# Optimization experiments

Hardware: AMD Instinct MI355X
Metric: run time of the kernel (lower is better)

The kernel has to match this reference:

```python
import jax, jax.numpy as jnp
import numpy as np

B, K, W, H = 32, 64, 100, 150
ALPHA = 0.2        # leaky-relu slope
THRES = 2e-4       # causal threshold


def setup_inputs() -> dict:
    ks = jax.random.split(jax.random.key(0), 20)
    s = 0.1
    inp = {
        "x": jax.random.normal(ks[0], (B, K, W), jnp.float32),
        "y": jax.random.normal(ks[1], (B, K, 1), jnp.float32),
        "z_noise": jax.random.normal(ks[2], (B, H), jnp.float32),
        "lin_w": jax.random.normal(ks[3], (W, W), jnp.float32) * s,
        "lin_b": jax.random.normal(ks[4], (W,), jnp.float32) * s,
        "a": jax.random.normal(ks[5], (2, 1), jnp.float32),
        "bias": jax.random.normal(ks[6], (K, K * W), jnp.float32) * 0.01,
        "gl_wih": jax.random.normal(ks[7], (3 * H, W), jnp.float32) * s,
        "gl_whh": jax.random.normal(ks[8], (3 * H, H), jnp.float32) * s,
        "gl_bih": jax.random.normal(ks[9], (3 * H,), jnp.float32) * s,
        "gl_bhh": jax.random.normal(ks[10], (3 * H,), jnp.float32) * s,
        "mu_w": jax.random.normal(ks[11], (H, H), jnp.float32) * s,
        "mu_b": jax.random.normal(ks[12], (H,), jnp.float32) * s,
        "std_w": jax.random.normal(ks[13], (H, H), jnp.float32) * s,
        "std_b": jax.random.normal(ks[14], (H,), jnp.float32) * s,
        "net_wih": jax.random.normal(ks[15], (K, 3 * H, W), jnp.float32) * s,
        "net_whh": jax.random.normal(ks[16], (K, 3 * H, H), jnp.float32) * s,
        "net_bih": jax.random.normal(ks[17], (K, 3 * H), jnp.float32) * s,
        "net_bhh": jax.random.normal(ks[18], (K, 3 * H), jnp.float32) * s,
    }
    return inp


def _gru_last(wih, whh, bih, bhh, xs, h0):
    # xs: [B, S, in], h0: [B, H] -> final hidden [B, H]. PyTorch gate order r,z,n.
    gx = jnp.einsum('bsi,gi->sbg', xs, wih) + bih  # [S, B, 3H]
    h_dim = h0.shape[-1]

    def step(h, g):
        gh = h @ whh.T + bhh
        r = jax.nn.sigmoid(g[:, :h_dim] + gh[:, :h_dim])
        z = jax.nn.sigmoid(g[:, h_dim:2 * h_dim] + gh[:, h_dim:2 * h_dim])
        n = jnp.tanh(g[:, 2 * h_dim:] + r * gh[:, 2 * h_dim:])
        return (1.0 - z) * n + z * h, None

    h_last, _ = jax.lax.scan(step, h0, gx)
    return h_last


def reference(x, y, z_noise, lin_w, lin_b, a, bias, gl_wih, gl_whh, gl_bih, gl_bhh,
              mu_w, mu_b, std_w, std_b, net_wih, net_whh, net_bih, net_bhh):
    xw = x[:, :, -W:]
    Wx = xw @ lin_w.T + lin_b                       # [B, K, W]
    v = Wx.reshape(Wx.shape[0], K * W)              # [B, K*W]
    # e = a_input @ a, where a_input[...,0]=y broadcast, a_input[...,1]=v tiled per node
    e = a[0, 0] * y + a[1, 0] * v[:, None, :] + bias  # [B, K, K*W]
    e = jax.nn.leaky_relu(e, ALPHA)
    attention = jax.nn.softmax(e, axis=2)           # dropout p=0 -> identity
    A = attention >= THRES                           # [B, K, K*W] mask
    Ax = jnp.where(A, v[:, None, :], 0.0)
    cause_x = Wx + Ax.sum(axis=2, keepdims=True)    # [B, K, W]
    # left GRU over the node dimension (seq len = K)
    h0 = jnp.zeros((cause_x.shape[0], H), cause_x.dtype)
    h_t = _gru_last(gl_wih, gl_whh, gl_bih, gl_bhh, cause_x, h0)  # [B, H]
    mu = h_t @ mu_w.T + mu_b
    log_var = h_t @ std_w.T + std_b
    sigma = jnp.exp(0.5 * log_var)
    z = mu + sigma * z_noise                        # [B, H]
    # K independent GRUs, same input Wx and same init state z -> vmap over weights
    causes = jax.vmap(lambda wi, wh, bi, bh: _gru_last(wi, wh, bi, bh, Wx, z))(
        net_wih, net_whh, net_bih, net_bhh)         # [K, B, H]
    return causes.transpose(1, 0, 2)                # [B, K, H]
```

## Files before the change

### kernel.cpp

```cpp
#include <hip/hip_runtime.h>

#define Bc 32
#define Kc 64
#define Wc 100
#define Hc 150
#define H3c 450
#define KWc 6400
#define ALPHAc 0.2f
#define THRESc 0.0002f

typedef unsigned int u32;
typedef unsigned short u16;
typedef __attribute__((ext_vector_type(8))) short short8;
typedef __attribute__((ext_vector_type(4))) float floatx4;

#define OFF_WX      0u
#define OFF_CS      204800u
#define OFF_GX      206848u
#define OFF_HT      1128448u
#define OFF_Z       1133248u

__device__ __forceinline__ float us2f(u16 u){ u32 x=((u32)u)<<16; return __uint_as_float(x); }
__device__ __forceinline__ u16 f2us(float f){
  u32 x = __float_as_uint(f);
  u32 r = (x + 0x7fffu + ((x>>16)&1u)) >> 16;
  return (u16)r;
}

__device__ __forceinline__ void lds_barrier(){
  __builtin_amdgcn_sched_barrier(0);
  asm volatile("s_waitcnt lgkmcnt(0)" ::: "memory");
  __builtin_amdgcn_s_barrier();
  __builtin_amdgcn_sched_barrier(0);
}

__global__ void wx_kernel(const float* __restrict__ x, const float* __restrict__ lin_w,
                          const float* __restrict__ lin_b, float* __restrict__ ws){
  int o = blockIdx.x*256 + threadIdx.x;
  if (o >= Bc*KWc) return;
  int i = o % Wc;
  int bk = o / Wc;
  const float4* xr = (const float4*)(x + bk*Wc);
  const float4* wr = (const float4*)(lin_w + i*Wc);
  float acc = lin_b[i];
  #pragma unroll
  for (int j=0;j<25;j++){
    float4 xv = xr[j], wv = wr[j];
    acc += xv.x*wv.x + xv.y*wv.y + xv.z*wv.z + xv.w*wv.w;
  }
  ws[OFF_WX + o] = acc;
}

__global__ void attn_kernel(const float* __restrict__ y, const float* __restrict__ a,
                            const float* __restrict__ bias, float* __restrict__ ws){
  __shared__ __align__(16) float e_l[KWc];
  __shared__ float red[4];
  int row = blockIdx.x;
  int b = row >> 6, k = row & 63;
  int tid = threadIdx.x;
  float a0 = a[0], a1 = a[1];
  float yv = y[row];
  const float4* v4  = (const float4*)(ws + OFF_WX + (size_t)b*KWc);
  const float4* br4 = (const float4*)(bias + (size_t)k*KWc);
  float4* e4 = (float4*)e_l;
  float ay = a0*yv;
  float m = -3.4e38f;
  for (int j=tid; j<KWc/4; j+=256){
    float4 vv = v4[j], bb = br4[j];
    float4 e;
    e.x = ay + a1*vv.x + bb.x; e.x = (e.x>=0.f)?e.x:ALPHAc*e.x;
    e.y = ay + a1*vv.y + bb.y; e.y = (e.y>=0.f)?e.y:ALPHAc*e.y;
    e.z = ay + a1*vv.z + bb.z; e.z = (e.z>=0.f)?e.z:ALPHAc*e.z;
    e.w = ay + a1*vv.w + bb.w; e.w = (e.w>=0.f)?e.w:ALPHAc*e.w;
    e4[j] = e;
    m = fmaxf(m, fmaxf(fmaxf(e.x,e.y), fmaxf(e.z,e.w)));
  }
  for (int o=32;o;o>>=1) m = fmaxf(m, __shfl_down(m, o));
  if ((tid&63)==0) red[tid>>6] = m;
  __syncthreads();
  m = fmaxf(fmaxf(red[0],red[1]), fmaxf(red[2],red[3]));
  __syncthreads();
  float ssum = 0.f;
  for (int j=tid; j<KWc/4; j+=256){
    float4 e = e4[j];
    ssum += __expf(e.x-m) + __expf(e.y-m) + __expf(e.z-m) + __expf(e.w-m);
  }
  for (int o=32;o;o>>=1) ssum += __shfl_down(ssum, o);
  if ((tid&63)==0) red[tid>>6] = ssum;
  __syncthreads();
  float s = red[0]+red[1]+red[2]+red[3];
  float thr = m + logf(THRESc * s);
  float cs = 0.f;
  for (int j=tid; j<KWc/4; j+=256){
    float4 e = e4[j];
    float4 vv = v4[j];
    if (e.x >= thr) cs += vv.x;
    if (e.y >= thr) cs += vv.y;
    if (e.z >= thr) cs += vv.z;
    if (e.w >= thr) cs += vv.w;
  }
  for (int o=32;o;o>>=1) cs += __shfl_down(cs, o);
  if ((tid&63)==0) red[tid>>6] = cs;
  __syncthreads();
  if (tid==0) ws[OFF_CS + row] = red[0]+red[1]+red[2]+red[3];
}

__global__ void glproj_kernel(const float* __restrict__ gl_wih, const float* __restrict__ gl_bih,
                              float* __restrict__ ws){
  int o = blockIdx.x*256 + threadIdx.x;
  if (o >= Kc*Bc*H3c) return;
  int g = o % H3c;
  int t = o / H3c;
  int b = t & 31, s = t >> 5;
  float cs = ws[OFF_CS + b*Kc + s];
  const float4* xr = (const float4*)(ws + OFF_WX + b*KWc + s*Wc);
  const float4* wr = (const float4*)(gl_wih + g*Wc);
  float acc = gl_bih[g];
  #pragma unroll
  for (int j=0;j<25;j++){
    float4 wv = wr[j], xv = xr[j];
    acc += (xv.x+cs)*wv.x + (xv.y+cs)*wv.y + (xv.z+cs)*wv.z + (xv.w+cs)*wv.w;
  }
  ws[OFF_GX + o] = acc;
}

__global__ void __launch_bounds__(512,1) glgru4_kernel(
    const float* __restrict__ gl_whh, const float* __restrict__ gl_bhh,
    float* __restrict__ ws){
  __shared__ __align__(16) float hbuf[2][152];
  __shared__ float dotb[3*152];
  int b = blockIdx.x;
  int tid = threadIdx.x;
  bool dotter = (tid < 450);
  int g = dotter ? tid/150 : 0;
  int t = dotter ? (tid - g*150) : 0;

  u32 wreg[75];
  {
    const float* wr = gl_whh + (size_t)(g*Hc + t)*Hc;
    #pragma unroll
    for (int k2=0;k2<75;k2++){
      float2 wv = dotter ? *(const float2*)(wr + 2*k2) : make_float2(0.f,0.f);
      wreg[k2] = (u32)f2us(wv.x) | ((u32)f2us(wv.y) << 16);
    }
  }
  if (tid < 152){ hbuf[0][tid] = 0.f; hbuf[1][tid] = 0.f; }

  float bh_r=0.f, bh_z=0.f, bh_n=0.f, hreg=0.f;
  if (tid < Hc){
    bh_r = gl_bhh[tid]; bh_z = gl_bhh[Hc+tid]; bh_n = gl_bhh[2*Hc+tid];
  }
  __syncthreads();

  for (int s=0;s<Kc;s++){
    int rb = s & 1;
    float gxr=0.f, gxz=0.f, gxn=0.f;
    if (tid < Hc){
      const float* gp = ws + OFF_GX + (size_t)(s*Bc + b)*H3c;
      gxr = gp[tid]; gxz = gp[Hc+tid]; gxn = gp[2*Hc+tid];
    }
    if (dotter){
      const float* hb = hbuf[rb];
      float a0=0.f, a1=0.f, a2=0.f;
      #pragma unroll
      for (int k2=0;k2<75;k2+=3){
        u32 u0 = wreg[k2], u1 = wreg[k2+1], u2 = wreg[k2+2];
        float2 h0 = *(const float2*)(hb + 2*k2);
        float2 h1 = *(const float2*)(hb + 2*k2+2);
        float2 h2 = *(const float2*)(hb + 2*k2+4);
        a0 += __uint_as_float(u0<<16)*h0.x + __uint_as_float(u0&0xffff0000u)*h0.y;
        a1 += __uint_as_float(u1<<16)*h1.x + __uint_as_float(u1&0xffff0000u)*h1.y;
        a2 += __uint_as_float(u2<<16)*h2.x + __uint_as_float(u2&0xffff0000u)*h2.y;
      }
      dotb[g*152 + t] = a0 + a1 + a2;
    }
    lds_barrier();
    if (tid < Hc){
      float a_r = gxr + dotb[tid]       + bh_r;
      float a_z = gxz + dotb[152+tid]   + bh_z;
      float dn  =       dotb[304+tid]   + bh_n;
      float rr = 1.f/(1.f+__expf(-a_r));
      float zz = 1.f/(1.f+__expf(-a_z));
      float nx = gxn + rr*dn;
      nx = fminf(fmaxf(nx,-15.f),15.f);
      float e2 = __expf(2.f*nx);
      float n = (e2-1.f)/(e2+1.f);
      float h = (1.f-zz)*n + zz*hreg;
      hreg = h;
      hbuf[rb^1][tid] = h;
    }
    lds_barrier();
  }
  if (tid < Hc) ws[OFF_HT + (size_t)b*Hc + tid] = hreg;
}

__global__ void z_kernel(const float* __restrict__ z_noise, const float* __restrict__ mu_w,
                         const float* __restrict__ mu_b, const float* __restrict__ std_w,
                         const float* __restrict__ std_b, float* __restrict__ ws){
  int o = blockIdx.x*256 + threadIdx.x;
  if (o >= Bc*Hc) return;
  int t = o % Hc, b = o / Hc;
  const float* h = ws + OFF_HT + b*Hc;
  const float2* mwr = (const float2*)(mu_w + t*Hc);
  const float2* swr = (const float2*)(std_w + t*Hc);
  float mu = mu_b[t], lv = std_b[t];
  for (int j=0;j<Hc/2;j++){
    float2 mw = mwr[j], sw = swr[j];
    float h0 = h[2*j], h1 = h[2*j+1];
    mu += h0*mw.x + h1*mw.y;
    lv += h0*sw.x + h1*sw.y;
  }
  float sg = expf(0.5f*lv);
  ws[OFF_Z + o] = mu + sg*z_noise[o];
}

__global__ void __launch_bounds__(512,1) causes3_kernel(
    const float* __restrict__ net_wih, const float* __restrict__ net_whh,
    const float* __restrict__ net_bih, const float* __restrict__ net_bhh,
    const float* __restrict__ ws, float* __restrict__ out){
  __shared__ __align__(16) u16 bF[9*16*40];
  __shared__ float g_rz[320*10];
  __shared__ float g_nh[160*10];
  __shared__ float g_np[160*10];
  int kk = blockIdx.x & 63, bg = blockIdx.x >> 6, b0 = bg*8;
  int tid = threadIdx.x;
  int w = tid >> 6, lane = tid & 63, quad = lane >> 4, n16 = lane & 15;
  const float* whhk = net_whh + (size_t)kk*H3c*Hc;
  const float* wihk = net_wih + (size_t)kk*H3c*Wc;
  const float* bihk = net_bih + kk*H3c;
  const float* bhhk = net_bhh + kk*H3c;

  short8 whhA[4][5], wihA[4][4];
  #pragma unroll
  for (int ti=0; ti<4; ti++){
    int tile = w*4 + ti;
    int sec = tile/10;
    int sr = (tile - sec*10)*16 + n16;
    bool rowok = (tile < 30) && (sr < Hc);
    int grow = (sec<3 ? sec : 2)*Hc + sr;
    #pragma unroll
    for (int c=0;c<5;c++){
      union { short8 v; u16 u[8]; } t8;
      #pragma unroll
      for (int j=0;j<8;j++){
        int k = c*32 + quad*8 + j;
        float v = (rowok && k < Hc) ? whhk[(size_t)grow*Hc + k] : 0.f;
        t8.u[j] = f2us(v);
      }
      whhA[ti][c] = t8.v;
    }
    #pragma unroll
    for (int c=0;c<4;c++){
      union { short8 v; u16 u[8]; } t8;
      #pragma unroll
      for (int j=0;j<8;j++){
        int k = c*32 + quad*8 + j;
        float v = (rowok && k < Wc) ? wihk[(size_t)grow*Wc + k] : 0.f;
        t8.u[j] = f2us(v);
      }
      wihA[ti][c] = t8.v;
    }
  }

  for (int i=tid; i<9*16*40/2; i+=512) ((u32*)bF)[i] = 0u;

  float hst[3] = {0.f,0.f,0.f};
  float brz_r[3], brz_z[3], bnh_[3], bnp_[3];
  #pragma unroll
  for (int q=0;q<3;q++){
    int task = tid + q*512;
    if (task < 1200){
      int t = task >> 3, bb = task & 7;
      float h = ws[OFF_Z + (b0+bb)*Hc + t];
      hst[q] = h;
      brz_r[q] = bhhk[t]      + bihk[t];
      brz_z[q] = bhhk[Hc+t]   + bihk[Hc+t];
      bnh_[q]  = bhhk[2*Hc+t];
      bnp_[q]  = bihk[2*Hc+t];
      u16 hi = f2us(h); float hif = us2f(hi); u16 lo = f2us(h - hif);
      bF[(t>>5)*640 + bb*40 + (t&31)] = hi;
      bF[(t>>5)*640 + (bb+8)*40 + (t&31)] = lo;
    }
  }
  for (int it=tid; it<800; it+=512){
    int bb = it/100, i = it - bb*100;
    float xv = ws[OFF_WX + (b0+bb)*KWc + i];
    bF[(5+(i>>5))*640 + bb*40 + (i&31)] = f2us(xv);
  }

  int bb0 = tid/100, i0 = tid - bb0*100;
  int it1 = tid + 512;
  int bb1 = it1/100, i1 = it1 - bb1*100;
  bool v1ok = (it1 < 800);

  const bool isN = (w >= 5);
  for (int s=0;s<Kc;s++){
    float xp0 = 0.f, xp1 = 0.f;
    if (s < Kc-1){
      xp0 = ws[OFF_WX + (size_t)(b0+bb0)*KWc + (s+1)*Wc + i0];
      if (v1ok) xp1 = ws[OFF_WX + (size_t)(b0+bb1)*KWc + (s+1)*Wc + i1];
    }
    lds_barrier();
    const u16* bBase = bF + (size_t)n16*40 + (size_t)quad*8;
    short8 bx[4];
    #pragma unroll
    for (int c=0;c<4;c++) bx[c] = *(const short8*)(bBase + (size_t)(5+c)*640);
    short8 bh[5];
    #pragma unroll
    for (int c=0;c<5;c++) bh[c] = *(const short8*)(bBase + (size_t)c*640);
    floatx4 acc[4] = {{0.f,0.f,0.f,0.f},{0.f,0.f,0.f,0.f},{0.f,0.f,0.f,0.f},{0.f,0.f,0.f,0.f}};
    #pragma unroll
    for (int ca=0;ca<4;ca++){
      #pragma unroll
      for (int ti=0;ti<4;ti++)
        acc[ti] = __builtin_amdgcn_mfma_f32_16x16x32_bf16(wihA[ti][ca], bx[ca], acc[ti], 0,0,0);
    }
    if (isN){
      if (n16 < 8){
        #pragma unroll
        for (int ti=0;ti<4;ti++){
          int tile = w*4 + ti;
          if (tile < 30){
            int srb = (tile - 20)*16 + quad*4;
            float* gq = g_np + srb*10 + n16;
            #pragma unroll
            for (int r=0;r<4;r++) gq[r*10] = acc[ti][r];
          }
        }
      }
      #pragma unroll
      for (int ti=0;ti<4;ti++) acc[ti] = (floatx4){0.f,0.f,0.f,0.f};
    }
    #pragma unroll
    for (int c=0;c<5;c++){
      #pragma unroll
      for (int ti=0;ti<4;ti++)
        acc[ti] = __builtin_amdgcn_mfma_f32_16x16x32_bf16(whhA[ti][c], bh[c], acc[ti], 0,0,0);
    }
    #pragma unroll
    for (int ti=0;ti<4;ti++){
      #pragma unroll
      for (int r=0;r<4;r++) acc[ti][r] += __shfl_xor(acc[ti][r], 8);
    }
    if (n16 < 8){
      #pragma unroll
      for (int ti=0;ti<4;ti++){
        int tile = w*4 + ti;
        if (tile < 30){
          int sec = tile/10;
          int srb = (tile - sec*10)*16 + quad*4;
          if (sec < 2){
            float* gp = g_rz + (sec*160 + srb)*10 + n16;
            #pragma unroll
            for (int r=0;r<4;r++) gp[r*10] = acc[ti][r];
          } else {
            float* gh = g_nh + srb*10 + n16;
            #pragma unroll
            for (int r=0;r<4;r++) gh[r*10] = acc[ti][r];
          }
        }
      }
    }
    lds_barrier();
    #pragma unroll
    for (int q=0;q<3;q++){
      int task = tid + q*512;
      if (task < 1200){
        int t = task >> 3, bb = task & 7;
        float a_r = g_rz[t*10+bb] + brz_r[q];
        float a_z = g_rz[(160+t)*10+bb] + brz_z[q];
        float r  = 1.f/(1.f+__expf(-a_r));
        float zz = 1.f/(1.f+__expf(-a_z));
        float nx = (g_np[t*10+bb] + bnp_[q]) + r*(g_nh[t*10+bb] + bnh_[q]);
        nx = fminf(fmaxf(nx,-15.f),15.f);
        float e2 = __expf(2.f*nx);
        float n = (e2-1.f)/(e2+1.f);
        float h = (1.f-zz)*n + zz*hst[q];
        hst[q] = h;
        u16 hi = f2us(h); float hif = us2f(hi); u16 lo = f2us(h - hif);
        bF[(t>>5)*640 + bb*40 + (t&31)] = hi;
        bF[(t>>5)*640 + (bb+8)*40 + (t&31)] = lo;
      }
    }
    if (s < Kc-1){
      bF[(5+(i0>>5))*640 + bb0*40 + (i0&31)] = f2us(xp0);
      if (v1ok) bF[(5+(i1>>5))*640 + bb1*40 + (i1&31)] = f2us(xp1);
    }
  }
  #pragma unroll
  for (int q=0;q<3;q++){
    int task = tid + q*512;
    if (task < 1200){
      int t = task >> 3, bb = task & 7;
      out[((size_t)(b0+bb)*Kc + kk)*Hc + t] = hst[q];
    }
  }
}

extern "C" void kernel_launch(void* const* d_in, const int* in_sizes, int n_in,
                              void* d_out, int out_size, void* d_ws, size_t ws_size,
                              hipStream_t stream){
  const float* x        = (const float*)d_in[0];
  const float* y        = (const float*)d_in[1];
  const float* z_noise  = (const float*)d_in[2];
  const float* lin_w    = (const float*)d_in[3];
  const float* lin_b    = (const float*)d_in[4];
  const float* a        = (const float*)d_in[5];
  const float* bias     = (const float*)d_in[6];
  const float* gl_wih   = (const float*)d_in[7];
  const float* gl_whh   = (const float*)d_in[8];
  const float* gl_bih   = (const float*)d_in[9];
  const float* gl_bhh   = (const float*)d_in[10];
  const float* mu_w     = (const float*)d_in[11];
  const float* mu_b     = (const float*)d_in[12];
  const float* std_w    = (const float*)d_in[13];
  const float* std_b    = (const float*)d_in[14];
  const float* net_wih  = (const float*)d_in[15];
  const float* net_whh  = (const float*)d_in[16];
  const float* net_bih  = (const float*)d_in[17];
  const float* net_bhh  = (const float*)d_in[18];
  float* ws = (float*)d_ws;
  float* out = (float*)d_out;

  wx_kernel<<<(Bc*KWc+255)/256, 256, 0, stream>>>(x, lin_w, lin_b, ws);
  attn_kernel<<<Bc*Kc, 256, 0, stream>>>(y, a, bias, ws);
  glproj_kernel<<<(Kc*Bc*H3c+255)/256, 256, 0, stream>>>(gl_wih, gl_bih, ws);
  glgru4_kernel<<<Bc, 512, 0, stream>>>(gl_whh, gl_bhh, ws);
  z_kernel<<<(Bc*Hc+255)/256, 256, 0, stream>>>(z_noise, mu_w, mu_b, std_w, std_b, ws);
  causes3_kernel<<<Kc*4, 512, 0, stream>>>(net_wih, net_whh, net_bih, net_bhh, ws, out);
}
```

Baseline: 483.8 us.

## Split left-GRU recurrent dot across 1024 threads and fuse z projection

The left GRU kernel now uses 900 active threads, so each hidden-row dot product is split into two halves that are summed through LDS. Its recurrent weights are kept in fp32 registers instead of packed bf16. The mu/log-var projection and reparameterisation are folded into the end of the same kernel, which removes the separate z_kernel launch. Shorter per-step dot chains should cut latency in the 64-step serial loop, at the cost of more threads, more registers per thread and an extra LDS add per gate.

```diff
diff --git a/kernel.cpp b/kernel.cpp
--- a/kernel.cpp
+++ b/kernel.cpp
@@ -124,25 +124,30 @@
   ws[OFF_GX + o] = acc;
 }
 
-__global__ void __launch_bounds__(512,1) glgru4_kernel(
+__global__ void __launch_bounds__(1024,1) glgru4_kernel(
     const float* __restrict__ gl_whh, const float* __restrict__ gl_bhh,
-    float* __restrict__ ws){
+    const float* __restrict__ z_noise, const float* __restrict__ mu_w,
+    const float* __restrict__ mu_b, const float* __restrict__ std_w,
+    const float* __restrict__ std_b, float* __restrict__ ws){
   __shared__ __align__(16) float hbuf[2][152];
-  __shared__ float dotb[3*152];
+  __shared__ __align__(16) float dotb[2][3][152];
   int b = blockIdx.x;
   int tid = threadIdx.x;
-  bool dotter = (tid < 450);
-  int g = dotter ? tid/150 : 0;
-  int t = dotter ? (tid - g*150) : 0;
-
-  u32 wreg[75];
-  {
-    const float* wr = gl_whh + (size_t)(g*Hc + t)*Hc;
-    #pragma unroll
-    for (int k2=0;k2<75;k2++){
-      float2 wv = dotter ? *(const float2*)(wr + 2*k2) : make_float2(0.f,0.f);
-      wreg[k2] = (u32)f2us(wv.x) | ((u32)f2us(wv.y) << 16);
-    }
+  bool dotter = (tid < 900);
+  int half = (tid >= 450) ? 1 : 0;
+  int row  = dotter ? (tid - half*450) : 0;
+  int g = row/150, t = row - g*150;
+
+  float wreg[76];
+  if (dotter){
+    const float* wr = gl_whh + (size_t)row*Hc + half*76;
+    #pragma unroll
+    for (int i=0;i<37;i++){
+      float2 v = *(const float2*)(wr + 2*i);
+      wreg[2*i] = v.x; wreg[2*i+1] = v.y;
+    }
+    if (!half){ float2 v = *(const float2*)(wr + 74); wreg[74]=v.x; wreg[75]=v.y; }
+    else      { wreg[74]=0.f; wreg[75]=0.f; }
   }
   if (tid < 152){ hbuf[0][tid] = 0.f; hbuf[1][tid] = 0.f; }
 
@@ -160,28 +165,28 @@
       gxr = gp[tid]; gxz = gp[Hc+tid]; gxn = gp[2*Hc+tid];
     }
     if (dotter){
-      const float* hb = hbuf[rb];
-      float a0=0.f, a1=0.f, a2=0.f;
-      #pragma unroll
-      for (int k2=0;k2<75;k2+=3){
-        u32 u0 = wreg[k2], u1 = wreg[k2+1], u2 = wreg[k2+2];
-        float2 h0 = *(const float2*)(hb + 2*k2);
-        float2 h1 = *(const float2*)(hb + 2*k2+2);
-        float2 h2 = *(const float2*)(hb + 2*k2+4);
-        a0 += __uint_as_float(u0<<16)*h0.x + __uint_as_float(u0&0xffff0000u)*h0.y;
-        a1 += __uint_as_float(u1<<16)*h1.x + __uint_as_float(u1&0xffff0000u)*h1.y;
-        a2 += __uint_as_float(u2<<16)*h2.x + __uint_as_float(u2&0xffff0000u)*h2.y;
-      }
-      dotb[g*152 + t] = a0 + a1 + a2;
+      const float* hb = &hbuf[rb][half*76];
+      float a0=0.f,a1=0.f,a2=0.f,a3=0.f;
+      #pragma unroll
+      for (int i=0;i<19;i++){
+        float4 h4 = *(const float4*)(hb + 4*i);
+        a0 += wreg[4*i]  *h4.x;
+        a1 += wreg[4*i+1]*h4.y;
+        a2 += wreg[4*i+2]*h4.z;
+        a3 += wreg[4*i+3]*h4.w;
+      }
+      dotb[half][g][t] = (a0+a1)+(a2+a3);
     }
     lds_barrier();
     if (tid < Hc){
-      float a_r = gxr + dotb[tid]       + bh_r;
-      float a_z = gxz + dotb[152+tid]   + bh_z;
-      float dn  =       dotb[304+tid]   + bh_n;
+      float dr = dotb[0][0][tid] + dotb[1][0][tid];
+      float dz = dotb[0][1][tid] + dotb[1][1][tid];
+      float dn = dotb[0][2][tid] + dotb[1][2][tid];
+      float a_r = gxr + dr + bh_r;
+      float a_z = gxz + dz + bh_z;
       float rr = 1.f/(1.f+__expf(-a_r));
       float zz = 1.f/(1.f+__expf(-a_z));
-      float nx = gxn + rr*dn;
+      float nx = gxn + rr*(dn + bh_n);
       nx = fminf(fmaxf(nx,-15.f),15.f);
       float e2 = __expf(2.f*nx);
       float n = (e2-1.f)/(e2+1.f);
@@ -192,26 +197,26 @@
     lds_barrier();
   }
   if (tid < Hc) ws[OFF_HT + (size_t)b*Hc + tid] = hreg;
-}
-
-__global__ void z_kernel(const float* __restrict__ z_noise, const float* __restrict__ mu_w,
-                         const float* __restrict__ mu_b, const float* __restrict__ std_w,
-                         const float* __restrict__ std_b, float* __restrict__ ws){
-  int o = blockIdx.x*256 + threadIdx.x;
-  if (o >= Bc*Hc) return;
-  int t = o % Hc, b = o / Hc;
-  const float* h = ws + OFF_HT + b*Hc;
-  const float2* mwr = (const float2*)(mu_w + t*Hc);
-  const float2* swr = (const float2*)(std_w + t*Hc);
-  float mu = mu_b[t], lv = std_b[t];
-  for (int j=0;j<Hc/2;j++){
-    float2 mw = mwr[j], sw = swr[j];
-    float h0 = h[2*j], h1 = h[2*j+1];
-    mu += h0*mw.x + h1*mw.y;
-    lv += h0*sw.x + h1*sw.y;
-  }
-  float sg = expf(0.5f*lv);
-  ws[OFF_Z + o] = mu + sg*z_noise[o];
+
+  if (tid < 300){
+    int which = tid/150, tt = tid - which*150;
+    const float* wrow = (which ? std_w : mu_w) + (size_t)tt*Hc;
+    float acc = which ? std_b[tt] : mu_b[tt];
+    const float* hb = hbuf[0];
+    #pragma unroll
+    for (int i=0;i<75;i++){
+      float2 wv = *(const float2*)(wrow + 2*i);
+      float2 hv = *(const float2*)(hb + 2*i);
+      acc += wv.x*hv.x + wv.y*hv.y;
+    }
+    dotb[0][which][tt] = acc;
+  }
+  lds_barrier();
+  if (tid < Hc){
+    float mu = dotb[0][0][tid], lv = dotb[0][1][tid];
+    float sg = expf(0.5f*lv);
+    ws[OFF_Z + (size_t)b*Hc + tid] = mu + sg*z_noise[(size_t)b*Hc + tid];
+  }
 }
 
 __global__ void __launch_bounds__(512,1) causes3_kernel(
@@ -425,7 +430,6 @@
   wx_kernel<<<(Bc*KWc+255)/256, 256, 0, stream>>>(x, lin_w, lin_b, ws);
   attn_kernel<<<Bc*Kc, 256, 0, stream>>>(y, a, bias, ws);
   glproj_kernel<<<(Kc*Bc*H3c+255)/256, 256, 0, stream>>>(gl_wih, gl_bih, ws);
-  glgru4_kernel<<<Bc, 512, 0, stream>>>(gl_whh, gl_bhh, ws);
-  z_kernel<<<(Bc*Hc+255)/256, 256, 0, stream>>>(z_noise, mu_w, mu_b, std_w, std_b, ws);
+  glgru4_kernel<<<Bc, 1024, 0, stream>>>(gl_whh, gl_bhh, z_noise, mu_w, mu_b, std_w, std_b, ws);
   causes3_kernel<<<Kc*4, 512, 0, stream>>>(net_wih, net_whh, net_bih, net_bhh, ws, out);
 }
```

After: 449.2 us. 7.1% less time.
